# Performance work log

Measured on AMD Instinct MI355X. Metric: run time of the kernel, lower is better.

The kernel has to match this reference:

```python
import jax, jax.numpy as jnp
import numpy as np

HEADS = 8
DIM_HEAD = 64
EPS = 1e-5


def _layernorm(x, g, b):
    m = jnp.mean(x, axis=-1, keepdims=True)
    v = jnp.mean((x - m) ** 2, axis=-1, keepdims=True)
    return (x - m) * jax.lax.rsqrt(v + EPS) * g + b


def setup_inputs() -> dict:
    key = jax.random.key(0)
    ks = jax.random.split(key, 8)
    b, c, hh, ww = 4, 256, 48, 48
    inner = HEADS * DIM_HEAD  # 512
    s = 0.02
    return {
        "x": jax.random.normal(ks[0], (b, c, hh, ww), jnp.float32),
        "Wq": jax.random.normal(ks[1], (c, inner), jnp.float32) * s,
        "Wk": jax.random.normal(ks[2], (c, inner), jnp.float32) * s,
        "Wv": jax.random.normal(ks[3], (c, inner), jnp.float32) * s,
        "Wo": jax.random.normal(ks[4], (inner, c), jnp.float32) * s,
        "bo": jnp.zeros((c,), jnp.float32),
        "g1": jnp.ones((c,), jnp.float32),
        "b1": jnp.zeros((c,), jnp.float32),
        "g2": jnp.ones((c,), jnp.float32),
        "b2": jnp.zeros((c,), jnp.float32),
        "Wf1": jax.random.normal(ks[5], (c, 2 * c), jnp.float32) * s,
        "bf1": jnp.zeros((2 * c,), jnp.float32),
        "Wf2": jax.random.normal(ks[6], (2 * c, c), jnp.float32) * s,
        "bf2": jnp.zeros((c,), jnp.float32),
        "Wp": jax.random.normal(ks[7], (c, c), jnp.float32) * s,
        "bp": jnp.zeros((c,), jnp.float32),
    }


def reference(x, Wq, Wk, Wv, Wo, bo, g1, b1, g2, b2, Wf1, bf1, Wf2, bf2, Wp, bp):
    b, c, hh, ww = x.shape
    n = hh * ww
    scale = DIM_HEAD ** -0.5
    x_in = x
    t = jnp.transpose(x.reshape(b, c, n), (0, 2, 1))  # [b, n, c]

    # --- CrossAttention (self-attn, context=None) ---
    tn = _layernorm(t, g1, b1)
    q = (tn @ Wq).reshape(b, n, HEADS, DIM_HEAD)
    k = (tn @ Wk).reshape(b, n, HEADS, DIM_HEAD)
    v = (tn @ Wv).reshape(b, n, HEADS, DIM_HEAD)
    sim = jnp.einsum("bihd,bjhd->bhij", q, k) * scale  # [b,h,n,n]
    attn = jax.nn.softmax(sim, axis=-1)
    o = jnp.einsum("bhij,bjhd->bihd", attn, v).reshape(b, n, HEADS * DIM_HEAD)
    t = o @ Wo + bo + t

    # --- FeedForward: Linear -> GELU(exact) -> Linear ---
    f = jax.nn.gelu(_layernorm(t, g2, b2) @ Wf1 + bf1, approximate=False)
    t = f @ Wf2 + bf2 + t

    # back to image and 1x1 conv (Wp[c_in, c_out])
    xi = jnp.transpose(t, (0, 2, 1)).reshape(b, c, hh, ww)
    y = jnp.einsum("bchw,co->bohw", xi, Wp) + bp[None, :, None, None]
    return y + x_in
```

## Files before the change

kernel.cpp:

```cpp
#include <hip/hip_runtime.h>
#include <math.h>

#define B_    4
#define C_    256
#define N_    2304
#define H_    8
#define DH_   64
#define IN_   512
#define ROWS_ 9216
#define NHALF 576

typedef __attribute__((ext_vector_type(8))) short short8;
typedef __attribute__((ext_vector_type(4))) float f32x4;
typedef __attribute__((ext_vector_type(16))) float f32x16;

__device__ __forceinline__ unsigned short f2bf(float f) {
    unsigned int u = __float_as_uint(f);
    u += 0x7fffu + ((u >> 16) & 1u);
    return (unsigned short)(u >> 16);
}

__device__ __forceinline__ float bf2f(unsigned short u) {
    return __uint_as_float(((unsigned)u) << 16);
}

__device__ __forceinline__ float gelu_exact(float x) {
    return 0.5f * x * (1.0f + erff(x * 0.70710678118654752440f));
}

__device__ __forceinline__ unsigned cvtpk(float lo, float hi) {
    unsigned r;
    asm("v_cvt_pk_bf16_f32 %0, %1, %2" : "=v"(r) : "v"(lo), "v"(hi));
    return r;
}

__device__ __forceinline__ void gload_lds16(const void* g, void* l) {
    __builtin_amdgcn_global_load_lds(
        (const __attribute__((address_space(1))) unsigned int*)g,
        (__attribute__((address_space(3))) unsigned int*)l, 16, 0, 0);
}

__device__ __forceinline__ const short8* frg(const short* base, int row, int chunk) {
    return (const short8*)(base + (row << 6) + (((chunk) ^ (row & 7)) << 3));
}

__device__ __forceinline__ int swz2(int row) {
    return (row & 7) ^ ((row >> 3) & 3);
}
__device__ __forceinline__ const short8* frg2(const short* base, int row, int chunk) {
    return (const short8*)(base + (row << 6) + (((chunk) ^ swz2(row)) << 3));
}

__global__ __launch_bounds__(256)
void k_pre(const float* __restrict__ Wq, const float* __restrict__ Wk,
           const float* __restrict__ Wv, const float* __restrict__ Wo,
           const float* __restrict__ Wf1, const float* __restrict__ Wf2,
           const float* __restrict__ Wp,
           unsigned short* Wqh, unsigned short* Wkh, unsigned short* Wvh,
           unsigned short* Woh, unsigned short* Wf1h, unsigned short* Wf2h,
           unsigned short* Wph,
           const float* __restrict__ x, float* __restrict__ T,
           unsigned short* __restrict__ TNh,
           const float* __restrict__ g1, const float* __restrict__ b1) {
    __shared__ float tile[32][257];
    int bid = blockIdx.x;
    int tid = threadIdx.x;
    if (bid < 1792) {
        int wz = bid >> 8;
        int rem = bid & 255;
        int nBase = (rem & 15) * 32;
        int kBase = (rem >> 4) * 32;
        const float* src; unsigned short* dst; int K, N;
        switch (wz) {
            case 0: src = Wq;  dst = Wqh;  K = 256; N = 512; break;
            case 1: src = Wk;  dst = Wkh;  K = 256; N = 512; break;
            case 2: src = Wv;  dst = Wvh;  K = 256; N = 512; break;
            case 3: src = Wo;  dst = Woh;  K = 512; N = 256; break;
            case 4: src = Wf1; dst = Wf1h; K = 256; N = 512; break;
            case 5: src = Wf2; dst = Wf2h; K = 512; N = 256; break;
            default: src = Wp; dst = Wph;  K = 256; N = 256; break;
        }
        if (nBase >= N || kBase >= K) return;
        float scl = (wz == 0) ? 0.18033688f : 1.0f;
        int tx = tid & 31, ty = tid >> 5;
        #pragma unroll
        for (int i = 0; i < 32; i += 8)
            tile[ty + i][tx] = src[(size_t)(kBase + ty + i) * N + nBase + tx];
        __syncthreads();
        #pragma unroll
        for (int i = 0; i < 32; i += 8)
            dst[(size_t)(nBase + ty + i) * K + kBase + tx] = f2bf(tile[tx][ty + i] * scl);
    } else {
        int idx = bid - 1792;
        int bb = idx / 72;
        int nBase = (idx - bb * 72) * 32;
        int tx = tid & 31;
        int tg = tid >> 5;
        const float* xp = x + (size_t)bb * C_ * N_ + nBase + tx;
        #pragma unroll
        for (int i = 0; i < 32; ++i) {
            int c = tg * 32 + i;
            tile[tx][c] = xp[(size_t)c * N_];
        }
        __syncthreads();
        int w = tid >> 6, lane = tid & 63;
        float g0 = g1[lane], ga = g1[lane + 64], gb2 = g1[lane + 128], gc = g1[lane + 192];
        float b0 = b1[lane], ba = b1[lane + 64], bb2 = b1[lane + 128], bc = b1[lane + 192];
        #pragma unroll
        for (int r8 = 0; r8 < 8; ++r8) {
            int row = w * 8 + r8;
            float v0 = tile[row][lane],       v1 = tile[row][lane + 64];
            float v2 = tile[row][lane + 128], v3 = tile[row][lane + 192];
            float s = v0 + v1 + v2 + v3;
            #pragma unroll
            for (int m = 1; m < 64; m <<= 1) s += __shfl_xor(s, m);
            float mean = s * (1.0f / C_);
            float d0 = v0 - mean, d1 = v1 - mean, d2 = v2 - mean, d3 = v3 - mean;
            float s2 = d0 * d0 + d1 * d1 + d2 * d2 + d3 * d3;
            #pragma unroll
            for (int m = 1; m < 64; m <<= 1) s2 += __shfl_xor(s2, m);
            float rs = rsqrtf(s2 * (1.0f / C_) + 1e-5f);
            size_t o = (size_t)(bb * N_ + nBase + row) * C_ + lane;
            T[o]       = v0; T[o + 64]  = v1; T[o + 128] = v2; T[o + 192] = v3;
            TNh[o]       = f2bf(d0 * rs * g0 + b0);
            TNh[o + 64]  = f2bf(d1 * rs * ga + ba);
            TNh[o + 128] = f2bf(d2 * rs * gb2 + bb2);
            TNh[o + 192] = f2bf(d3 * rs * gc + bc);
        }
    }
}

__global__ __launch_bounds__(256)
void k_layernorm_bf16(const float* __restrict__ in, unsigned short* __restrict__ out,
                      const float* __restrict__ g, const float* __restrict__ b) {
    int wv = threadIdx.x >> 6;
    int lane = threadIdx.x & 63;
    int row = blockIdx.x * 4 + wv;
    float4 v = ((const float4*)(in + (size_t)row * C_))[lane];
    float s = v.x + v.y + v.z + v.w;
    #pragma unroll
    for (int m = 1; m < 64; m <<= 1) s += __shfl_xor(s, m);
    float mean = s * (1.0f / C_);
    float dx = v.x - mean, dy = v.y - mean, dz = v.z - mean, dw = v.w - mean;
    float s2 = dx * dx + dy * dy + dz * dz + dw * dw;
    #pragma unroll
    for (int m = 1; m < 64; m <<= 1) s2 += __shfl_xor(s2, m);
    float rs = rsqrtf(s2 * (1.0f / C_) + 1e-5f);
    float4 gv = ((const float4*)g)[lane];
    float4 bv = ((const float4*)b)[lane];
    ushort4 o;
    o.x = f2bf(dx * rs * gv.x + bv.x);
    o.y = f2bf(dy * rs * gv.y + bv.y);
    o.z = f2bf(dz * rs * gv.z + bv.z);
    o.w = f2bf(dw * rs * gv.w + bv.w);
    *(ushort4*)(out + (size_t)row * C_ + lane * 4) = o;
}

template <int EP>
__global__ __launch_bounds__(256)
void k_gemm64(const short* __restrict__ A, const short* __restrict__ Bt,
              void* __restrict__ Out, const float* __restrict__ bias,
              const float* __restrict__ Res, int M, int N, int K) {
    __shared__ __align__(16) short As[64 * 64];
    __shared__ __align__(16) short Bs[64 * 64];
    int tid = threadIdx.x;
    int w = tid >> 6;
    int lane = tid & 63;
    int l15 = lane & 15;
    int lg = lane >> 4;
    int wr = w >> 1, wc = w & 1;
    int rowBase = blockIdx.y * 64;
    int colBase = blockIdx.x * 64;

    f32x4 acc[2][2];
    #pragma unroll
    for (int m = 0; m < 2; ++m)
        #pragma unroll
        for (int n = 0; n < 2; ++n) acc[m][n] = (f32x4){0.f, 0.f, 0.f, 0.f};

    for (int k0 = 0; k0 < K; k0 += 64) {
        __syncthreads();
        #pragma unroll
        for (int a = 0; a < 2; ++a) {
            int rr = (w << 4) + (a << 3) + (lane >> 3);
            int cc = (lane & 7) ^ (lane >> 3);
            gload_lds16(A + (size_t)(rowBase + rr) * K + k0 + cc * 8,
                        As + (((w << 4) + (a << 3)) << 6));
            gload_lds16(Bt + (size_t)(colBase + rr) * K + k0 + cc * 8,
                        Bs + (((w << 4) + (a << 3)) << 6));
        }
        asm volatile("s_waitcnt vmcnt(0)" ::: "memory");
        __syncthreads();
        short8 af[2][2], bf[2][2];
        #pragma unroll
        for (int m = 0; m < 2; ++m) {
            af[m][0] = *frg(As, wr * 32 + m * 16 + l15, lg);
            af[m][1] = *frg(As, wr * 32 + m * 16 + l15, 4 + lg);
        }
        #pragma unroll
        for (int n = 0; n < 2; ++n) {
            bf[n][0] = *frg(Bs, wc * 32 + n * 16 + l15, lg);
            bf[n][1] = *frg(Bs, wc * 32 + n * 16 + l15, 4 + lg);
        }
        #pragma unroll
        for (int m = 0; m < 2; ++m)
            #pragma unroll
            for (int n = 0; n < 2; ++n) {
                acc[m][n] = __builtin_amdgcn_mfma_f32_16x16x32_bf16(af[m][0], bf[n][0], acc[m][n], 0, 0, 0);
                acc[m][n] = __builtin_amdgcn_mfma_f32_16x16x32_bf16(af[m][1], bf[n][1], acc[m][n], 0, 0, 0);
            }
    }

    int arB = rowBase + wr * 32;
    int brB = colBase + wc * 32;
    int bb = 0;
    if (EP == 5) bb = brB / N_;
    #pragma unroll
    for (int m = 0; m < 2; ++m) {
        #pragma unroll
        for (int i = 0; i < 4; ++i) {
            int ar = arB + m * 16 + lg * 4 + i;
            #pragma unroll
            for (int n = 0; n < 2; ++n) {
                int br = brB + n * 16 + l15;
                float v = acc[m][n][i];
                if constexpr (EP == 2) {
                    size_t o = (size_t)ar * N + br;
                    ((float*)Out)[o] = v + bias[br] + Res[o];
                } else if constexpr (EP == 3) {
                    ((unsigned short*)Out)[(size_t)ar * N + br] = f2bf(gelu_exact(v + bias[br]));
                } else if constexpr (EP == 4) {
                    size_t o = (size_t)ar * N + br;
                    ((unsigned short*)Out)[o] = f2bf(v + bias[br] + Res[o]);
                } else {
                    size_t o = ((size_t)(bb * C_) + ar) * N_ + (br - bb * N_);
                    ((float*)Out)[o] = v + bias[ar] + Res[o];
                }
            }
        }
    }
}

__global__ __launch_bounds__(256)
void k_gemm_qkv(const short* __restrict__ TNh, const short* __restrict__ Wqh,
                const short* __restrict__ Wkh, const short* __restrict__ Wvh,
                unsigned short* __restrict__ Qb, unsigned short* __restrict__ Kb,
                unsigned short* __restrict__ Vt) {
    __shared__ __align__(16) short As[64 * 64];
    __shared__ __align__(16) short Bs[64 * 64];
    int bid = blockIdx.x;
    int z = bid / 1152;
    int rem = bid - z * 1152;
    int tid = threadIdx.x;
    int w = tid >> 6;
    int lane = tid & 63;
    int l15 = lane & 15;
    int lg = lane >> 4;
    int wr = w >> 1, wc = w & 1;
    const short *A, *Bt;
    int rowBase, colBase;
    if (z < 2) {
        A = TNh; Bt = z ? Wkh : Wqh;
        colBase = (rem & 7) * 64;
        rowBase = (rem >> 3) * 64;
    } else {
        A = Wvh; Bt = TNh;
        colBase = (rem % 144) * 64;
        rowBase = (rem / 144) * 64;
    }
    const int K = C_;

    f32x4 acc[2][2];
    #pragma unroll
    for (int m = 0; m < 2; ++m)
        #pragma unroll
        for (int n = 0; n < 2; ++n) acc[m][n] = (f32x4){0.f, 0.f, 0.f, 0.f};

    for (int k0 = 0; k0 < K; k0 += 64) {
        __syncthreads();
        #pragma unroll
        for (int a = 0; a < 2; ++a) {
            int rr = (w << 4) + (a << 3) + (lane >> 3);
            int cc = (lane & 7) ^ (lane >> 3);
            gload_lds16(A + (size_t)(rowBase + rr) * K + k0 + cc * 8,
                        As + (((w << 4) + (a << 3)) << 6));
            gload_lds16(Bt + (size_t)(colBase + rr) * K + k0 + cc * 8,
                        Bs + (((w << 4) + (a << 3)) << 6));
        }
        asm volatile("s_waitcnt vmcnt(0)" ::: "memory");
        __syncthreads();
        short8 af[2][2], bf[2][2];
        #pragma unroll
        for (int m = 0; m < 2; ++m) {
            af[m][0] = *frg(As, wr * 32 + m * 16 + l15, lg);
            af[m][1] = *frg(As, wr * 32 + m * 16 + l15, 4 + lg);
        }
        #pragma unroll
        for (int n = 0; n < 2; ++n) {
            bf[n][0] = *frg(Bs, wc * 32 + n * 16 + l15, lg);
            bf[n][1] = *frg(Bs, wc * 32 + n * 16 + l15, 4 + lg);
        }
        #pragma unroll
        for (int m = 0; m < 2; ++m)
            #pragma unroll
            for (int n = 0; n < 2; ++n) {
                acc[m][n] = __builtin_amdgcn_mfma_f32_16x16x32_bf16(af[m][0], bf[n][0], acc[m][n], 0, 0, 0);
                acc[m][n] = __builtin_amdgcn_mfma_f32_16x16x32_bf16(af[m][1], bf[n][1], acc[m][n], 0, 0, 0);
            }
    }

    int arB = rowBase + wr * 32;
    int brB = colBase + wc * 32;
    if (z < 2) {
        unsigned short* Out = z ? Kb : Qb;
        #pragma unroll
        for (int m = 0; m < 2; ++m)
            #pragma unroll
            for (int i = 0; i < 4; ++i) {
                int ar = arB + m * 16 + lg * 4 + i;
                #pragma unroll
                for (int n = 0; n < 2; ++n)
                    Out[(size_t)ar * IN_ + brB + n * 16 + l15] = f2bf(acc[m][n][i]);
            }
    } else {
        int bb = brB / N_;
        #pragma unroll
        for (int m = 0; m < 2; ++m)
            #pragma unroll
            for (int i = 0; i < 4; ++i) {
                int ar = arB + m * 16 + lg * 4 + i;
                #pragma unroll
                for (int n = 0; n < 2; ++n) {
                    int br = brB + n * 16 + l15;
                    Vt[((size_t)(bb * IN_) + ar) * N_ + (br - bb * N_)] = f2bf(acc[m][n][i]);
                }
            }
    }
}

__global__ __launch_bounds__(256, 3)
void k_flash_mfma(const short* __restrict__ Qb, const short* __restrict__ Kb,
                  const short* __restrict__ Vt,
                  unsigned short* O0, unsigned short* O1,
                  unsigned short* O2, unsigned short* O3,
                  float* __restrict__ Lsum) {
    __shared__ __align__(16) short Ks[64 * 64];
    __shared__ __align__(16) short Vs[64 * 64];
    int tid = threadIdx.x;
    int lane = tid & 63;
    int l31 = lane & 31;
    int h5 = lane >> 5;
    int w = tid >> 6;

    int logical = (blockIdx.x & 7) * 288 + (blockIdx.x >> 3);
    int pair = logical / 18;
    int qi = logical - pair * 18;
    int bh = pair & 31;
    int half = pair >> 5;
    int bb = bh >> 3, h = bh & 7;
    int qBase = qi * 128;
    int h0 = half * NHALF;

    const short* Qp = Qb + ((size_t)bb * N_ + qBase + w * 32) * IN_ + h * DH_;
    const short* Kp = Kb + (size_t)bb * N_ * IN_ + h * DH_;
    const short* Vp = Vt + ((size_t)bb * IN_ + h * DH_) * N_;

    short8 qf[4];
    #pragma unroll
    for (int kk = 0; kk < 4; ++kk)
        qf[kk] = *(const short8*)(Qp + (size_t)l31 * IN_ + kk * 16 + h5 * 8);

    short8 ones;
    #pragma unroll
    for (int j = 0; j < 8; ++j) ones[j] = (short)0x3F80;

    int r0s = tid >> 3, c0s = tid & 7;
    int r1s = (tid + 256) >> 3, c1s = tid & 7;
    int w0s = (c0s ^ swz2(r0s)) << 3;
    int w1s = (c1s ^ swz2(r1s)) << 3;
    uint4 kreg0 = *(const uint4*)(Kp + (size_t)(h0 + r0s) * IN_ + c0s * 8);
    uint4 kreg1 = *(const uint4*)(Kp + (size_t)(h0 + r1s) * IN_ + c1s * 8);
    uint4 vreg0 = *(const uint4*)(Vp + (size_t)r0s * N_ + h0 + c0s * 8);
    uint4 vreg1 = *(const uint4*)(Vp + (size_t)r1s * N_ + h0 + c1s * 8);

    f32x16 oacc0 = (f32x16)(0.0f);
    f32x16 oacc1 = (f32x16)(0.0f);
    f32x16 lacc  = (f32x16)(0.0f);

    for (int kt = h0; kt < h0 + NHALF; kt += 64) {
        __syncthreads();
        *(uint4*)(Ks + (r0s << 6) + w0s) = kreg0;
        *(uint4*)(Ks + (r1s << 6) + w1s) = kreg1;
        *(uint4*)(Vs + (r0s << 6) + w0s) = vreg0;
        *(uint4*)(Vs + (r1s << 6) + w1s) = vreg1;
        __syncthreads();
        if (kt + 64 < h0 + NHALF) {
            kreg0 = *(const uint4*)(Kp + (size_t)(kt + 64 + r0s) * IN_ + c0s * 8);
            kreg1 = *(const uint4*)(Kp + (size_t)(kt + 64 + r1s) * IN_ + c1s * 8);
            vreg0 = *(const uint4*)(Vp + (size_t)r0s * N_ + kt + 64 + c0s * 8);
            vreg1 = *(const uint4*)(Vp + (size_t)r1s * N_ + kt + 64 + c1s * 8);
        }

        short8 pa[4];
        #pragma unroll
        for (int s = 0; s < 2; ++s) {
            f32x16 stv = (f32x16)(0.0f);
            __builtin_amdgcn_s_setprio(1);
            #pragma unroll
            for (int kk = 0; kk < 4; ++kk) {
                short8 kf = *frg2(Ks, s * 32 + l31, kk * 2 + h5);
                stv = __builtin_amdgcn_mfma_f32_32x32x16_bf16(kf, qf[kk], stv, 0, 0, 0);
            }
            __builtin_amdgcn_s_setprio(0);
            unsigned u[8];
            #pragma unroll
            for (int q = 0; q < 4; ++q) {
                u[2 * q]     = cvtpk(exp2f(stv[4 * q + 0]), exp2f(stv[4 * q + 1]));
                u[2 * q + 1] = cvtpk(exp2f(stv[4 * q + 2]), exp2f(stv[4 * q + 3]));
            }
            asm volatile("v_permlane32_swap_b32 %0, %1" : "+v"(u[0]), "+v"(u[2]));
            asm volatile("v_permlane32_swap_b32 %0, %1" : "+v"(u[1]), "+v"(u[3]));
            asm volatile("v_permlane32_swap_b32 %0, %1" : "+v"(u[4]), "+v"(u[6]));
            asm volatile("v_permlane32_swap_b32 %0, %1" : "+v"(u[5]), "+v"(u[7]));
            union { unsigned uu[4]; short8 s8; } c0, c1;
            c0.uu[0] = u[0]; c0.uu[1] = u[1]; c0.uu[2] = u[2]; c0.uu[3] = u[3];
            c1.uu[0] = u[4]; c1.uu[1] = u[5]; c1.uu[2] = u[6]; c1.uu[3] = u[7];
            pa[2 * s]     = c0.s8;
            pa[2 * s + 1] = c1.s8;
        }

        __builtin_amdgcn_s_setprio(1);
        #pragma unroll
        for (int kk = 0; kk < 4; ++kk) {
            short8 vf0 = *frg2(Vs, l31, kk * 2 + h5);
            short8 vf1 = *frg2(Vs, 32 + l31, kk * 2 + h5);
            lacc  = __builtin_amdgcn_mfma_f32_32x32x16_bf16(pa[kk], ones, lacc, 0, 0, 0);
            oacc0 = __builtin_amdgcn_mfma_f32_32x32x16_bf16(pa[kk], vf0, oacc0, 0, 0, 0);
            oacc1 = __builtin_amdgcn_mfma_f32_32x32x16_bf16(pa[kk], vf1, oacc1, 0, 0, 0);
        }
        __builtin_amdgcn_s_setprio(0);
    }

    unsigned short* OpH = (half == 0) ? O0 : (half == 1) ? O1 : (half == 2) ? O2 : O3;
    unsigned short* Op = OpH + ((size_t)bb * N_ + qBase + w * 32) * IN_ + h * DH_;
    #pragma unroll
    for (int reg = 0; reg < 16; ++reg) {
        int q = (reg & 3) + 8 * (reg >> 2) + 4 * h5;
        Op[(size_t)q * IN_ + l31]      = f2bf(oacc0[reg]);
        Op[(size_t)q * IN_ + 32 + l31] = f2bf(oacc1[reg]);
    }
    if (l31 == 0) {
        float* Lp = Lsum + (((size_t)half * B_ + bb) * H_ + h) * N_ + qBase + w * 32;
        #pragma unroll
        for (int reg = 0; reg < 16; ++reg) {
            int q = (reg & 3) + 8 * (reg >> 2) + 4 * h5;
            Lp[q] = lacc[reg];
        }
    }
}

__global__ __launch_bounds__(256)
void k_combine(const unsigned short* p0, const unsigned short* p1,
               const unsigned short* p2, const unsigned short* p3,
               const float* __restrict__ Lsum, unsigned short* Ob) {
    int wv = threadIdx.x >> 6;
    int lane = threadIdx.x & 63;
    int row = blockIdx.x * 4 + wv;
    int bb = row / N_;
    int n = row - bb * N_;
    int hh = lane >> 3;
    float l = 0.f;
    #pragma unroll
    for (int q4 = 0; q4 < 4; ++q4)
        l += Lsum[(((size_t)q4 * B_ + bb) * H_ + hh) * N_ + n];
    float inv = 1.0f / l;
    size_t off = (size_t)row * IN_ + lane * 8;
    short8 a0 = *(const short8*)(p0 + off);
    short8 a1 = *(const short8*)(p1 + off);
    short8 a2 = *(const short8*)(p2 + off);
    short8 a3 = *(const short8*)(p3 + off);
    unsigned short o[8];
    #pragma unroll
    for (int j = 0; j < 8; ++j)
        o[j] = f2bf((bf2f((unsigned short)a0[j]) + bf2f((unsigned short)a1[j]) +
                     bf2f((unsigned short)a2[j]) + bf2f((unsigned short)a3[j])) * inv);
    *(uint4*)(Ob + off) = *(uint4*)o;
}

extern "C" void kernel_launch(void* const* d_in, const int* in_sizes, int n_in,
                              void* d_out, int out_size, void* d_ws, size_t ws_size,
                              hipStream_t stream) {
    (void)in_sizes; (void)n_in; (void)out_size; (void)ws_size;
    const float* x   = (const float*)d_in[0];
    const float* Wq  = (const float*)d_in[1];
    const float* Wk  = (const float*)d_in[2];
    const float* Wv  = (const float*)d_in[3];
    const float* Wo  = (const float*)d_in[4];
    const float* bo  = (const float*)d_in[5];
    const float* g1  = (const float*)d_in[6];
    const float* b1  = (const float*)d_in[7];
    const float* g2  = (const float*)d_in[8];
    const float* b2  = (const float*)d_in[9];
    const float* Wf1 = (const float*)d_in[10];
    const float* bf1 = (const float*)d_in[11];
    const float* Wf2 = (const float*)d_in[12];
    const float* bf2 = (const float*)d_in[13];
    const float* Wp  = (const float*)d_in[14];
    const float* bp  = (const float*)d_in[15];
    float* out = (float*)d_out;
    float* ws  = (float*)d_ws;

    float* T    = ws;
    float* T2   = ws + 2359296;
    unsigned short* TNh = (unsigned short*)(ws + 4718592);
    short* Qb   = (short*)(ws + 5898240);
    short* Kb   = (short*)(ws + 8257536);
    short* Vt   = (short*)(ws + 10616832);
    unsigned short* Obh = (unsigned short*)(ws + 12976128);
    short* F    = (short*)(ws + 15335424);
    short* T3h  = (short*)(ws + 17694720);
    unsigned short* Wqh  = (unsigned short*)(ws + 18874368);
    unsigned short* Wkh  = (unsigned short*)(ws + 18939904);
    unsigned short* Wvh  = (unsigned short*)(ws + 19005440);
    unsigned short* Woh  = (unsigned short*)(ws + 19070976);
    unsigned short* Wf1h = (unsigned short*)(ws + 19136512);
    unsigned short* Wf2h = (unsigned short*)(ws + 19202048);
    unsigned short* Wph  = (unsigned short*)(ws + 19267584);
    unsigned short* Op0  = (unsigned short*)(ws + 19398656);
    unsigned short* Op3  = (unsigned short*)(ws + 21757952);
    unsigned short* Op1  = Obh;
    unsigned short* Op2  = (unsigned short*)F;
    float* Lsum = ws + 24117248;

    k_pre<<<dim3(2080), 256, 0, stream>>>(Wq, Wk, Wv, Wo, Wf1, Wf2, Wp,
                                          Wqh, Wkh, Wvh, Woh, Wf1h, Wf2h, Wph,
                                          x, T, TNh, g1, b1);
    k_gemm_qkv<<<dim3(3456), 256, 0, stream>>>((const short*)TNh, (const short*)Wqh,
                                               (const short*)Wkh, (const short*)Wvh,
                                               (unsigned short*)Qb, (unsigned short*)Kb,
                                               (unsigned short*)Vt);
    k_flash_mfma<<<dim3(2304), 256, 0, stream>>>(Qb, Kb, Vt, Op0, Op1, Op2, Op3, Lsum);
    k_combine<<<2304, 256, 0, stream>>>(Op0, Op1, Op2, Op3, Lsum, Obh);
    k_gemm64<2><<<dim3(4, 144), 256, 0, stream>>>((const short*)Obh, (const short*)Woh, T2, bo, T, ROWS_, C_, IN_);
    k_layernorm_bf16<<<2304, 256, 0, stream>>>(T2, TNh, g2, b2);
    k_gemm64<3><<<dim3(8, 144), 256, 0, stream>>>((const short*)TNh, (const short*)Wf1h, F, bf1, nullptr, ROWS_, IN_, C_);
    k_gemm64<4><<<dim3(4, 144), 256, 0, stream>>>((const short*)F, (const short*)Wf2h, T3h, bf2, T2, ROWS_, C_, IN_);
    k_gemm64<5><<<dim3(144, 4), 256, 0, stream>>>((const short*)Wph, (const short*)T3h, out, bp, x, C_, ROWS_, C_);
}
```

Measured before the change: 151.9 us.

## Double-buffer flash K/V tiles with direct global-to-LDS loads

The flash attention kernel now stages K and V tiles straight into LDS using direct global-to-LDS loads into two alternating buffers. This drops the old register staging and the second barrier per iteration. The next tile's load is issued right after the barrier so it overlaps the MFMA work on the current tile. In exchange, LDS use doubles, which may lower occupancy at 3 blocks per CU, and the code relies on the gload_lds16 helper and its swizzle matching the frg2 reads.

After: 151.9 us. Within noise of the previous version (-0.0%).

```diff
diff --git a/kernel.cpp b/kernel.cpp
--- a/kernel.cpp
+++ b/kernel.cpp
@@ -344,8 +344,8 @@
                   unsigned short* O0, unsigned short* O1,
                   unsigned short* O2, unsigned short* O3,
                   float* __restrict__ Lsum) {
-    __shared__ __align__(16) short Ks[64 * 64];
-    __shared__ __align__(16) short Vs[64 * 64];
+    __shared__ __align__(16) short Ks[2][64 * 64];
+    __shared__ __align__(16) short Vs[2][64 * 64];
     int tid = threadIdx.x;
     int lane = tid & 63;
     int l31 = lane & 31;
@@ -374,32 +374,30 @@
     #pragma unroll
     for (int j = 0; j < 8; ++j) ones[j] = (short)0x3F80;
 
-    int r0s = tid >> 3, c0s = tid & 7;
-    int r1s = (tid + 256) >> 3, c1s = tid & 7;
-    int w0s = (c0s ^ swz2(r0s)) << 3;
-    int w1s = (c1s ^ swz2(r1s)) << 3;
-    uint4 kreg0 = *(const uint4*)(Kp + (size_t)(h0 + r0s) * IN_ + c0s * 8);
-    uint4 kreg1 = *(const uint4*)(Kp + (size_t)(h0 + r1s) * IN_ + c1s * 8);
-    uint4 vreg0 = *(const uint4*)(Vp + (size_t)r0s * N_ + h0 + c0s * 8);
-    uint4 vreg1 = *(const uint4*)(Vp + (size_t)r1s * N_ + h0 + c1s * 8);
+    auto STAGE = [&](int buf, int kt2) {
+        #pragma unroll
+        for (int j = 0; j < 2; ++j) {
+            int br = (w << 4) + (j << 3);
+            int rr = br + (lane >> 3);
+            int cc = (lane & 7) ^ (lane >> 3) ^ ((2 * w + j) & 3);
+            gload_lds16(Kp + (size_t)(kt2 + rr) * IN_ + cc * 8, &Ks[buf][br << 6]);
+            gload_lds16(Vp + (size_t)rr * N_ + kt2 + cc * 8, &Vs[buf][br << 6]);
+        }
+    };
 
     f32x16 oacc0 = (f32x16)(0.0f);
     f32x16 oacc1 = (f32x16)(0.0f);
     f32x16 lacc  = (f32x16)(0.0f);
 
-    for (int kt = h0; kt < h0 + NHALF; kt += 64) {
-        __syncthreads();
-        *(uint4*)(Ks + (r0s << 6) + w0s) = kreg0;
-        *(uint4*)(Ks + (r1s << 6) + w1s) = kreg1;
-        *(uint4*)(Vs + (r0s << 6) + w0s) = vreg0;
-        *(uint4*)(Vs + (r1s << 6) + w1s) = vreg1;
-        __syncthreads();
-        if (kt + 64 < h0 + NHALF) {
-            kreg0 = *(const uint4*)(Kp + (size_t)(kt + 64 + r0s) * IN_ + c0s * 8);
-            kreg1 = *(const uint4*)(Kp + (size_t)(kt + 64 + r1s) * IN_ + c1s * 8);
-            vreg0 = *(const uint4*)(Vp + (size_t)r0s * N_ + kt + 64 + c0s * 8);
-            vreg1 = *(const uint4*)(Vp + (size_t)r1s * N_ + kt + 64 + c1s * 8);
-        }
+    STAGE(0, h0);
+    const int NT = NHALF / 64;
+    for (int t = 0; t < NT; ++t) {
+        asm volatile("s_waitcnt vmcnt(0)" ::: "memory");
+        __builtin_amdgcn_s_barrier();
+        __builtin_amdgcn_sched_barrier(0);
+        if (t + 1 < NT) STAGE((t + 1) & 1, h0 + (t + 1) * 64);
+        const short* Kc = Ks[t & 1];
+        const short* Vc = Vs[t & 1];
 
         short8 pa[4];
         #pragma unroll
@@ -408,7 +406,7 @@
             __builtin_amdgcn_s_setprio(1);
             #pragma unroll
             for (int kk = 0; kk < 4; ++kk) {
-                short8 kf = *frg2(Ks, s * 32 + l31, kk * 2 + h5);
+                short8 kf = *frg2(Kc, s * 32 + l31, kk * 2 + h5);
                 stv = __builtin_amdgcn_mfma_f32_32x32x16_bf16(kf, qf[kk], stv, 0, 0, 0);
             }
             __builtin_amdgcn_s_setprio(0);
@@ -432,8 +430,8 @@
         __builtin_amdgcn_s_setprio(1);
         #pragma unroll
         for (int kk = 0; kk < 4; ++kk) {
-            short8 vf0 = *frg2(Vs, l31, kk * 2 + h5);
-            short8 vf1 = *frg2(Vs, 32 + l31, kk * 2 + h5);
+            short8 vf0 = *frg2(Vc, l31, kk * 2 + h5);
+            short8 vf1 = *frg2(Vc, 32 + l31, kk * 2 + h5);
             lacc  = __builtin_amdgcn_mfma_f32_32x32x16_bf16(pa[kk], ones, lacc, 0, 0, 0);
             oacc0 = __builtin_amdgcn_mfma_f32_32x32x16_bf16(pa[kk], vf0, oacc0, 0, 0, 0);
             oacc1 = __builtin_amdgcn_mfma_f32_32x32x16_bf16(pa[kk], vf1, oacc1, 0, 0, 0);
```
